# Performance work log

Hardware: AMD Instinct MI355X
Metric: run time of the kernel (lower is better)

Reference implementation:

```python
import jax, jax.numpy as jnp
import numpy as np

WINDOW = 128
BACKWARD = 1
FORWARD = 0

def look_around(x, pad_value):
    # x: [b, windows, window_size, ...]; pad window axis and gather shifted windows
    w = x.shape[1]
    pads = [(0, 0), (BACKWARD, FORWARD)] + [(0, 0)] * (x.ndim - 2)
    p = jnp.pad(x, pads, constant_values=pad_value)
    return jnp.concatenate([p[:, i:i + w] for i in range(BACKWARD + FORWARD + 1)], axis=2)

def setup_inputs() -> dict:
    key = jax.random.key(0)
    ks = jax.random.split(key, 5)
    shp = (2, 16, 4096, 64)
    names = ['q', 'k', 'q_rot', 'k_rot', 'v']
    inp = {n: jax.random.normal(ks[i], shp, dtype=jnp.float32) for i, n in enumerate(names)}
    inp['states'] = 0
    inp['inferring_states'] = 0
    return inp

def reference(q, k, q_rot, k_rot, v, states, inferring_states):
    shape = q.shape
    merge = lambda t: t.reshape(-1, t.shape[-2], t.shape[-1])
    q, k, q_rot, k_rot, v = map(merge, (q, k, q_rot, k_rot, v))
    b, t, e = q.shape
    windows = t // WINDOW
    ticker = jnp.arange(t, dtype=q.dtype)[None, :]
    b_t = ticker.reshape(1, windows, WINDOW)
    bucket = lambda x: x.reshape(b, windows, WINDOW, e)
    bq, bk, bq_rot, bk_rot, bv = map(bucket, (q, k, q_rot, k_rot, v))
    bk = look_around(bk, 0.0)
    bk_rot = look_around(bk_rot, 0.0)
    bv = look_around(bv, 0.0)
    bq_t = b_t
    bq_k = look_around(b_t, -1.0)
    scale = e ** (-0.5)
    dots = jnp.einsum('bwie,bwje->bwij', bq, bk) * scale
    dots_rot = jnp.einsum('bwie,bwje->bwij', bq_rot, bk_rot) * scale
    mask_value = -jnp.finfo(dots.dtype).max
    causal_mask = bq_t[:, :, :, None] < bq_k[:, :, None, :]
    pad_mask = bq_k[:, :, None, :] == -1
    mask = causal_mask | pad_mask
    dots = jnp.where(mask, mask_value, dots)
    dots_rot = jnp.where(mask, mask_value, dots_rot)
    attn = jax.nn.softmax(dots + dots_rot, axis=-1)
    out = jnp.einsum('bwij,bwje->bwie', attn, bv)
    return out.reshape(shape)
```

## Files before the change

kernel.cpp:

```cpp
#include <hip/hip_runtime.h>
#include <stdint.h>

#define T 4096
#define E 64
#define NBH 32
#define NWIN 32
#define LDK 136
#define LDV 72
#define LDP 72
#define KK_ELEMS (64*LDK)
#define VT_ELEMS (64*LDV)
#define BUF_ELEMS (KK_ELEMS+VT_ELEMS)
#define PW_ELEMS (16*LDP)
#define SMEM_BYTES ((2*BUF_ELEMS + 8*PW_ELEMS)*2)

typedef __attribute__((ext_vector_type(8))) short short8;
typedef __attribute__((ext_vector_type(4))) short short4v;
typedef __attribute__((ext_vector_type(4))) float f32x4;

__device__ __forceinline__ short f2bf(float x) {
  unsigned u = __float_as_uint(x);
  u += 0x7fffu + ((u >> 16) & 1u);
  return (short)(u >> 16);
}

__device__ __forceinline__ void block_sync_lds() {
  asm volatile("s_waitcnt lgkmcnt(0)" ::: "memory");
  __builtin_amdgcn_s_barrier();
  asm volatile("" ::: "memory");
}

struct SubStage { float4 sk[4]; float sv[8]; };

__device__ __forceinline__ void sub_issue(SubStage& st,
    const float* __restrict__ k, const float* __restrict__ kr,
    const float* __restrict__ v, size_t rowbase, int tid, int wid, int lane) {
#pragma unroll
  for (int m = 0; m < 2; ++m) {
    const float* src = m ? kr : k;
#pragma unroll
    for (int it = 0; it < 2; ++it) {
      int idx = it * 512 + tid;
      st.sk[m * 2 + it] = *(const float4*)(src + (rowbase + (idx >> 4)) * E + (idx & 15) * 4);
    }
  }
  const float* vp = v + (rowbase + wid * 8) * E + lane;
#pragma unroll
  for (int i = 0; i < 8; ++i) st.sv[i] = vp[(size_t)i * E];
}

__device__ __forceinline__ void sub_commit(const SubStage& st,
    short* __restrict__ KK, short* __restrict__ Vt, int tid, int wid, int lane) {
#pragma unroll
  for (int m = 0; m < 2; ++m)
#pragma unroll
    for (int it = 0; it < 2; ++it) {
      int idx = it * 512 + tid;
      float4 f = st.sk[m * 2 + it];
      short4v h = { f2bf(f.x), f2bf(f.y), f2bf(f.z), f2bf(f.w) };
      *(short4v*)(KK + (idx >> 4) * LDK + m * 64 + (idx & 15) * 4) = h;
    }
#pragma unroll
  for (int rq = 0; rq < 2; ++rq) {
    short4v h = { f2bf(st.sv[rq*4+0]), f2bf(st.sv[rq*4+1]),
                  f2bf(st.sv[rq*4+2]), f2bf(st.sv[rq*4+3]) };
    *(short4v*)(Vt + lane * LDV + wid * 8 + rq * 4) = h;
  }
}

__device__ __forceinline__ void q_issue(float4* sq,
    const float* __restrict__ q, const float* __restrict__ qr,
    size_t rbase, int w, int wid, int li, int lg) {
  const size_t qrow = rbase + (size_t)w * 128 + wid * 16 + li;
#pragma unroll
  for (int kt = 0; kt < 4; ++kt) {
    const float* sp = (kt < 2 ? q : qr) + qrow * E + (kt & 1) * 32 + lg * 8;
    sq[kt * 2 + 0] = *(const float4*)sp;
    sq[kt * 2 + 1] = *(const float4*)(sp + 4);
  }
}

__device__ __forceinline__ void q_commit(const float4* sq, short8* aF) {
#pragma unroll
  for (int kt = 0; kt < 4; ++kt) {
    float4 f0 = sq[kt * 2], f1 = sq[kt * 2 + 1];
    short8 a;
    a[0]=f2bf(f0.x*0.125f); a[1]=f2bf(f0.y*0.125f); a[2]=f2bf(f0.z*0.125f); a[3]=f2bf(f0.w*0.125f);
    a[4]=f2bf(f1.x*0.125f); a[5]=f2bf(f1.y*0.125f); a[6]=f2bf(f1.z*0.125f); a[7]=f2bf(f1.w*0.125f);
    aF[kt] = a;
  }
}

__global__ __launch_bounds__(512, 4)
void la_attn(const float* __restrict__ qg, const float* __restrict__ kg,
             const float* __restrict__ qrg, const float* __restrict__ krg,
             const float* __restrict__ vg, float* __restrict__ outg) {
  extern __shared__ short smem[];

  const int lid = blockIdx.y * NWIN + blockIdx.x;
  const int wl  = (lid & 7) * 128 + (lid >> 3);
  const int win = wl & (NWIN - 1), bh = wl >> 5;

  const int tid = threadIdx.x;
  const int wid = tid >> 6, lane = tid & 63;
  const int li = lane & 15, lg = lane >> 4;
  const size_t rbase = (size_t)bh * T;
  const int rowb = wid * 16 + lg * 4;

  short* PW = smem + 2 * BUF_ELEMS + wid * PW_ELEMS;
  const int pxor_w = lg << 4;
  const int pxor_r = (li >> 2) << 4;

  short8 aF[4];
  SubStage st;

  const int s0 = (win == 0) ? 2 : 0;
#define KROW(s) (rbase + (size_t)(win * 128 + ((s) - 2) * 64))

  {
    SubStage stA;
    float4 sq[8];
    sub_issue(stA, kg, krg, vg, KROW(s0), tid, wid, lane);
    q_issue(sq, qg, qrg, rbase, win, wid, li, lg);
    sub_commit(stA, smem, smem + KK_ELEMS, tid, wid, lane);
    q_commit(sq, aF);
    if (s0 + 1 < 4) sub_issue(st, kg, krg, vg, KROW(s0 + 1), tid, wid, lane);
  }
  block_sync_lds();

  float m[4], l[4];
  f32x4 O[4] = {{0,0,0,0},{0,0,0,0},{0,0,0,0},{0,0,0,0}};
#pragma unroll
  for (int r = 0; r < 4; ++r) { m[r] = -1e30f; l[r] = 0.f; }

  for (int s = s0; s < 4; ++s) {
    const int cur = (s - s0) & 1;
    short* KKc = smem + cur * BUF_ELEMS;
    short* Vtc = KKc + KK_ELEMS;

    if (s + 1 < 4) {
      sub_commit(st, smem + (cur ^ 1) * BUF_ELEMS,
                 smem + (cur ^ 1) * BUF_ELEMS + KK_ELEMS, tid, wid, lane);
      if (s + 2 < 4) sub_issue(st, kg, krg, vg, KROW(s + 2), tid, wid, lane);
      asm volatile("" ::: "memory");
    }

    f32x4 S[4];
#pragma unroll
    for (int ct = 0; ct < 4; ++ct) {
      f32x4 acc = {0.f, 0.f, 0.f, 0.f};
      const short* kb = KKc + (ct * 16 + li) * LDK + lg * 8;
#pragma unroll
      for (int kt = 0; kt < 4; ++kt)
        acc = __builtin_amdgcn_mfma_f32_16x16x32_bf16(aF[kt], *(const short8*)(kb + kt * 32), acc, 0, 0, 0);
      S[ct] = acc;
    }

    const bool causal = (s >= 2);
#pragma unroll
    for (int r = 0; r < 4; ++r) {
      const int qi = rowb + r;
      if (causal) {
#pragma unroll
        for (int ct = 0; ct < 4; ++ct) {
          int jj = (s - 2) * 64 + ct * 16 + li;
          if (jj > qi) S[ct][r] = -1e30f;
        }
      }
      float mx = fmaxf(fmaxf(S[0][r], S[1][r]), fmaxf(S[2][r], S[3][r]));
      mx = fmaxf(mx, __shfl_xor(mx, 1));
      mx = fmaxf(mx, __shfl_xor(mx, 2));
      mx = fmaxf(mx, __shfl_xor(mx, 4));
      mx = fmaxf(mx, __shfl_xor(mx, 8));
      float mn = fmaxf(m[r], mx);
      float f = __expf(m[r] - mn);
      float sm = 0.f;
#pragma unroll
      for (int ct = 0; ct < 4; ++ct) {
        float e = __expf(S[ct][r] - mn);
        S[ct][r] = e;
        sm += e;
      }
      sm += __shfl_xor(sm, 1);
      sm += __shfl_xor(sm, 2);
      sm += __shfl_xor(sm, 4);
      sm += __shfl_xor(sm, 8);
      l[r] = l[r] * f + sm;
      m[r] = mn;
#pragma unroll
      for (int nt = 0; nt < 4; ++nt) O[nt][r] *= f;
    }

#pragma unroll
    for (int cc = 0; cc < 4; ++cc)
#pragma unroll
      for (int r = 0; r < 4; ++r)
        PW[(lg * 4 + r) * LDP + ((cc * 16 + li) ^ pxor_w)] = f2bf(S[cc][r]);
#pragma unroll
    for (int kt = 0; kt < 2; ++kt) {
      short8 aP = *(const short8*)(PW + li * LDP + ((kt * 32 + lg * 8) ^ pxor_r));
#pragma unroll
      for (int nt = 0; nt < 4; ++nt) {
        short8 b = *(const short8*)(Vtc + (nt * 16 + li) * LDV + kt * 32 + lg * 8);
        O[nt] = __builtin_amdgcn_mfma_f32_16x16x32_bf16(aP, b, O[nt], 0, 0, 0);
      }
    }

    block_sync_lds();
  }

  float* op = outg + (rbase + (size_t)win * 128 + rowb) * E;
#pragma unroll
  for (int r = 0; r < 4; ++r) {
    float linv = 1.f / l[r];
#pragma unroll
    for (int nt = 0; nt < 4; ++nt)
      op[(size_t)r * E + nt * 16 + li] = O[nt][r] * linv;
  }
#undef KROW
}

extern "C" void kernel_launch(void* const* d_in, const int* in_sizes, int n_in,
                              void* d_out, int out_size, void* d_ws, size_t ws_size,
                              hipStream_t stream) {
  const float* q  = (const float*)d_in[0];
  const float* k  = (const float*)d_in[1];
  const float* qr = (const float*)d_in[2];
  const float* kr = (const float*)d_in[3];
  const float* v  = (const float*)d_in[4];
  float* out = (float*)d_out;
  la_attn<<<dim3(NWIN, NBH), 512, SMEM_BYTES, stream>>>(q, k, qr, kr, v, out);
}
```

Baseline: 209.9 us.

## Transpose MFMA operands to keep P in registers and XOR-swizzle LDS tiles

The kernel swaps the MFMA operand order so S^T is computed and each lane holds a full query row. Softmax reductions then need only two cross-lane shuffles instead of four per row. The probability tile goes from registers to the PV MFMA operand through packed bf16 conversion and lane shuffles, removing the per-wave LDS round trip for P. K and V^T tiles use unpadded XOR-swizzled layouts to avoid bank conflicts with less LDS, and output stores become float4. The price is a more complex shuffle and select sequence, with some risk of bank conflicts in the new swizzle.

```diff
diff --git a/kernel.cpp b/kernel.cpp
--- a/kernel.cpp
+++ b/kernel.cpp
@@ -5,14 +5,12 @@
 #define E 64
 #define NBH 32
 #define NWIN 32
-#define LDK 136
-#define LDV 72
-#define LDP 72
-#define KK_ELEMS (64*LDK)
-#define VT_ELEMS (64*LDV)
+#define LDKS 128
+#define LDVS 64
+#define KK_ELEMS (64*LDKS)
+#define VT_ELEMS (64*LDVS)
 #define BUF_ELEMS (KK_ELEMS+VT_ELEMS)
-#define PW_ELEMS (16*LDP)
-#define SMEM_BYTES ((2*BUF_ELEMS + 8*PW_ELEMS)*2)
+#define SMEM_BYTES (2*BUF_ELEMS*2)
 
 typedef __attribute__((ext_vector_type(8))) short short8;
 typedef __attribute__((ext_vector_type(4))) short short4v;
@@ -24,6 +22,12 @@
   return (short)(u >> 16);
 }
 
+__device__ __forceinline__ unsigned cvtpk(float lo, float hi) {
+  unsigned r;
+  asm("v_cvt_pk_bf16_f32 %0, %1, %2" : "=v"(r) : "v"(lo), "v"(hi));
+  return r;
+}
+
 __device__ __forceinline__ void block_sync_lds() {
   asm volatile("s_waitcnt lgkmcnt(0)" ::: "memory");
   __builtin_amdgcn_s_barrier();
@@ -56,15 +60,17 @@
 #pragma unroll
     for (int it = 0; it < 2; ++it) {
       int idx = it * 512 + tid;
+      int row = idx >> 4;
+      int chunk = m * 8 + ((idx & 15) >> 1);
       float4 f = st.sk[m * 2 + it];
       short4v h = { f2bf(f.x), f2bf(f.y), f2bf(f.z), f2bf(f.w) };
-      *(short4v*)(KK + (idx >> 4) * LDK + m * 64 + (idx & 15) * 4) = h;
+      *(short4v*)(KK + row * LDKS + ((chunk ^ (row & 15)) << 3) + (idx & 1) * 4) = h;
     }
 #pragma unroll
   for (int rq = 0; rq < 2; ++rq) {
     short4v h = { f2bf(st.sv[rq*4+0]), f2bf(st.sv[rq*4+1]),
                   f2bf(st.sv[rq*4+2]), f2bf(st.sv[rq*4+3]) };
-    *(short4v*)(Vt + lane * LDV + wid * 8 + rq * 4) = h;
+    *(short4v*)(Vt + lane * LDVS + ((wid ^ (lane & 7)) << 3) + rq * 4) = h;
   }
 }
 
@@ -105,11 +111,7 @@
   const int wid = tid >> 6, lane = tid & 63;
   const int li = lane & 15, lg = lane >> 4;
   const size_t rbase = (size_t)bh * T;
-  const int rowb = wid * 16 + lg * 4;
-
-  short* PW = smem + 2 * BUF_ELEMS + wid * PW_ELEMS;
-  const int pxor_w = lg << 4;
-  const int pxor_r = (li >> 2) << 4;
+  const int q_i = wid * 16 + li;
 
   short8 aF[4];
   SubStage st;
@@ -128,10 +130,8 @@
   }
   block_sync_lds();
 
-  float m[4], l[4];
+  float m = -1e30f, l = 0.f;
   f32x4 O[4] = {{0,0,0,0},{0,0,0,0},{0,0,0,0},{0,0,0,0}};
-#pragma unroll
-  for (int r = 0; r < 4; ++r) { m[r] = -1e30f; l[r] = 0.f; }
 
   for (int s = s0; s < 4; ++s) {
     const int cur = (s - s0) & 1;
@@ -145,77 +145,99 @@
       asm volatile("" ::: "memory");
     }
 
-    f32x4 S[4];
+    f32x4 p[4];
 #pragma unroll
     for (int ct = 0; ct < 4; ++ct) {
       f32x4 acc = {0.f, 0.f, 0.f, 0.f};
-      const short* kb = KKc + (ct * 16 + li) * LDK + lg * 8;
-#pragma unroll
-      for (int kt = 0; kt < 4; ++kt)
-        acc = __builtin_amdgcn_mfma_f32_16x16x32_bf16(aF[kt], *(const short8*)(kb + kt * 32), acc, 0, 0, 0);
-      S[ct] = acc;
-    }
-
-    const bool causal = (s >= 2);
-#pragma unroll
-    for (int r = 0; r < 4; ++r) {
-      const int qi = rowb + r;
-      if (causal) {
-#pragma unroll
-        for (int ct = 0; ct < 4; ++ct) {
-          int jj = (s - 2) * 64 + ct * 16 + li;
-          if (jj > qi) S[ct][r] = -1e30f;
-        }
+      const int row = ct * 16 + li;
+#pragma unroll
+      for (int kt = 0; kt < 4; ++kt) {
+        const short* kb = KKc + row * LDKS + (((kt * 4 + lg) ^ li) << 3);
+        acc = __builtin_amdgcn_mfma_f32_16x16x32_bf16(*(const short8*)kb, aF[kt], acc, 0, 0, 0);
       }
-      float mx = fmaxf(fmaxf(S[0][r], S[1][r]), fmaxf(S[2][r], S[3][r]));
-      mx = fmaxf(mx, __shfl_xor(mx, 1));
-      mx = fmaxf(mx, __shfl_xor(mx, 2));
-      mx = fmaxf(mx, __shfl_xor(mx, 4));
-      mx = fmaxf(mx, __shfl_xor(mx, 8));
-      float mn = fmaxf(m[r], mx);
-      float f = __expf(m[r] - mn);
-      float sm = 0.f;
-#pragma unroll
-      for (int ct = 0; ct < 4; ++ct) {
-        float e = __expf(S[ct][r] - mn);
-        S[ct][r] = e;
+      p[ct] = acc;
+    }
+
+    if (s >= 2) {
+      const int joff = (s - 2) * 64 + lg * 4;
+#pragma unroll
+      for (int ct = 0; ct < 4; ++ct)
+#pragma unroll
+        for (int r = 0; r < 4; ++r)
+          if (joff + ct * 16 + r > q_i) p[ct][r] = -1e30f;
+    }
+    float mx = -1e30f;
+#pragma unroll
+    for (int ct = 0; ct < 4; ++ct)
+#pragma unroll
+      for (int r = 0; r < 4; ++r) mx = fmaxf(mx, p[ct][r]);
+    mx = fmaxf(mx, __shfl_xor(mx, 16));
+    mx = fmaxf(mx, __shfl_xor(mx, 32));
+    const float mn = fmaxf(m, mx);
+    const float f = __expf(m - mn);
+    float sm = 0.f;
+#pragma unroll
+    for (int ct = 0; ct < 4; ++ct)
+#pragma unroll
+      for (int r = 0; r < 4; ++r) {
+        float e = __expf(p[ct][r] - mn);
+        p[ct][r] = e;
         sm += e;
       }
-      sm += __shfl_xor(sm, 1);
-      sm += __shfl_xor(sm, 2);
-      sm += __shfl_xor(sm, 4);
-      sm += __shfl_xor(sm, 8);
-      l[r] = l[r] * f + sm;
-      m[r] = mn;
-#pragma unroll
-      for (int nt = 0; nt < 4; ++nt) O[nt][r] *= f;
-    }
-
-#pragma unroll
-    for (int cc = 0; cc < 4; ++cc)
-#pragma unroll
-      for (int r = 0; r < 4; ++r)
-        PW[(lg * 4 + r) * LDP + ((cc * 16 + li) ^ pxor_w)] = f2bf(S[cc][r]);
+    sm += __shfl_xor(sm, 16);
+    sm += __shfl_xor(sm, 32);
+    l = l * f + sm;
+    m = mn;
+#pragma unroll
+    for (int nt = 0; nt < 4; ++nt)
+#pragma unroll
+      for (int r = 0; r < 4; ++r) O[nt][r] *= f;
+
+    unsigned W0[4], W1[4];
+#pragma unroll
+    for (int ct = 0; ct < 4; ++ct) {
+      W0[ct] = cvtpk(p[ct][0], p[ct][1]);
+      W1[ct] = cvtpk(p[ct][2], p[ct][3]);
+    }
+
+    const bool lowhalf = (lg < 2);
+    const bool sendR = (lg == 0) | (lg == 3);
 #pragma unroll
     for (int kt = 0; kt < 2; ++kt) {
-      short8 aP = *(const short8*)(PW + li * LDP + ((kt * 32 + lg * 8) ^ pxor_r));
+      const int cA = kt * 2, cB = cA + 1;
+      unsigned P0 = lowhalf ? W0[cB] : W0[cA];
+      unsigned P1 = lowhalf ? W1[cB] : W1[cA];
+      unsigned R0 = __shfl_xor(P0, 32);
+      unsigned R1 = __shfl_xor(P1, 32);
+      unsigned L0 = lowhalf ? W0[cA] : W0[cB];
+      unsigned L1 = lowhalf ? W1[cA] : W1[cB];
+      unsigned S0 = sendR ? R0 : L0;
+      unsigned S1 = sendR ? R1 : L1;
+      unsigned T0 = __shfl_xor(S0, 16);
+      unsigned T1 = __shfl_xor(S1, 16);
+      unsigned F0 = (lg == 0) ? L0 : ((lg == 2) ? R0 : T0);
+      unsigned F1 = (lg == 0) ? L1 : ((lg == 2) ? R1 : T1);
+      unsigned G0 = (lg == 1) ? R0 : ((lg == 3) ? L0 : T0);
+      unsigned G1 = (lg == 1) ? R1 : ((lg == 3) ? L1 : T1);
+      union { unsigned u[4]; short8 s; } bu;
+      bu.u[0] = F0; bu.u[1] = F1; bu.u[2] = G0; bu.u[3] = G1;
+      const short8 bP = bu.s;
 #pragma unroll
       for (int nt = 0; nt < 4; ++nt) {
-        short8 b = *(const short8*)(Vtc + (nt * 16 + li) * LDV + kt * 32 + lg * 8);
-        O[nt] = __builtin_amdgcn_mfma_f32_16x16x32_bf16(aP, b, O[nt], 0, 0, 0);
+        const short* vb = Vtc + (nt * 16 + li) * LDVS + (((kt * 4 + lg) ^ (li & 7)) << 3);
+        O[nt] = __builtin_amdgcn_mfma_f32_16x16x32_bf16(*(const short8*)vb, bP, O[nt], 0, 0, 0);
       }
     }
 
     block_sync_lds();
   }
 
-  float* op = outg + (rbase + (size_t)win * 128 + rowb) * E;
-#pragma unroll
-  for (int r = 0; r < 4; ++r) {
-    float linv = 1.f / l[r];
-#pragma unroll
-    for (int nt = 0; nt < 4; ++nt)
-      op[(size_t)r * E + nt * 16 + li] = O[nt][r] * linv;
+  const float linv = 1.f / l;
+  float* op = outg + (rbase + (size_t)win * 128 + wid * 16 + li) * E + lg * 4;
+#pragma unroll
+  for (int nt = 0; nt < 4; ++nt) {
+    float4 o = { O[nt][0] * linv, O[nt][1] * linv, O[nt][2] * linv, O[nt][3] * linv };
+    *(float4*)(op + nt * 16) = o;
   }
 #undef KROW
 }
```

Result: faster. 201.3 us (-4.1%).
